# Performance work log

Measured on AMD Instinct MI355X. Metric: run time of the kernel, lower is better.

## Reference

```python
import jax, jax.numpy as jnp
import numpy as np

EMBED = 1024
N_HEAD = 16
D_HID = EMBED // N_HEAD
R_FF = 4
D_FF = EMBED * R_FF
LN_EPS = 1e-5


def layer_norm(x, gamma, beta):
    mu = jnp.mean(x, axis=-1, keepdims=True)
    var = jnp.var(x, axis=-1, keepdims=True)
    return (x - mu) * jax.lax.rsqrt(var + LN_EPS) * gamma + beta


def setup_inputs() -> dict:
    key = jax.random.key(0)
    ks = jax.random.split(key, 10)
    B, S = 4, 2048
    # torch nn.Linear stores weight as [out, in]; y = x @ W.T
    def xavier(k, shape):
        fan_out, fan_in = shape
        lim = np.sqrt(6.0 / (fan_in + fan_out))
        return jax.random.uniform(k, shape, jnp.float32, -lim, lim)
    return {
        "x": jax.random.normal(ks[0], (B, S, EMBED), jnp.float32),
        "Wq": xavier(ks[1], (EMBED, EMBED)),
        "Wk": xavier(ks[2], (EMBED, EMBED)),
        "Wv": xavier(ks[3], (EMBED, EMBED)),
        "Wo": xavier(ks[4], (EMBED, EMBED)),
        "bo": jnp.zeros((EMBED,), jnp.float32),
        "ln1_g": jnp.ones((EMBED,), jnp.float32),
        "ln1_b": jnp.zeros((EMBED,), jnp.float32),
        "ln2_g": jnp.ones((EMBED,), jnp.float32),
        "ln2_b": jnp.zeros((EMBED,), jnp.float32),
        "W1": jax.random.normal(ks[5], (D_FF, EMBED), jnp.float32) * np.sqrt(2.0 / EMBED),
        "b1": jnp.zeros((D_FF,), jnp.float32),
        "W2": xavier(ks[6], (EMBED, D_FF)),
        "b2": jnp.zeros((EMBED,), jnp.float32),
    }


def reference(x, Wq, Wk, Wv, Wo, bo, ln1_g, ln1_b, ln2_g, ln2_b, W1, b1, W2, b2):
    B, S, E = x.shape
    scaling = 1.0 / np.sqrt(D_HID)
    # --- attention (pre-LN), dropout = identity (eval) ---
    xn = layer_norm(x, ln1_g, ln1_b)
    q = (xn @ Wq.T).reshape(B, S, N_HEAD, D_HID) * scaling
    k = (xn @ Wk.T).reshape(B, S, N_HEAD, D_HID)
    v = (xn @ Wv.T).reshape(B, S, N_HEAD, D_HID)
    scores = jnp.einsum("bqhd,bkhd->bhqk", q, k)
    attn = jax.nn.softmax(scores, axis=-1)
    out = jnp.einsum("bhqk,bkhd->bqhd", attn, v).reshape(B, S, E)
    out = out @ Wo.T + bo
    x = x + out
    # --- feed-forward (pre-LN) ---
    xn = layer_norm(x, ln2_g, ln2_b)
    h = jax.nn.relu(xn @ W1.T + b1)
    x = x + (h @ W2.T + b2)
    return x
```

## Files before the change

kernel.cpp:

```cpp
#include <hip/hip_runtime.h>
#include <hip/hip_bf16.h>
#include <cstdint>


typedef __attribute__((ext_vector_type(8))) short bf16x8;
typedef __attribute__((ext_vector_type(4))) float f32x4;

#define LDSAS __attribute__((address_space(3)))
#define GLBAS __attribute__((address_space(1)))

#define CQK 0.18033688011112044f

__device__ __forceinline__ unsigned short f2bf(float f) {
  union { float f; unsigned u; } c; c.f = f;
  unsigned u = c.u + 0x7fffu + ((c.u >> 16) & 1u);
  return (unsigned short)(u >> 16);
}

__device__ __forceinline__ unsigned pk2(float a, float b) {
  __hip_bfloat162 h = __float22bfloat162_rn(make_float2(a, b));
  union { __hip_bfloat162 h; unsigned u; } c; c.h = h; return c.u;
}

__device__ __forceinline__ void async16(const unsigned short* g, unsigned short* l) {
  __builtin_amdgcn_global_load_lds((const GLBAS unsigned int*)g,
                                   (LDSAS unsigned int*)l, 16, 0, 0);
}

__global__ void cvt_all(const float* __restrict__ q, const float* __restrict__ k,
                        const float* __restrict__ v, const float* __restrict__ o,
                        const float* __restrict__ w1, const float* __restrict__ w2,
                        unsigned short* __restrict__ wsb) {
  const long i = (long)blockIdx.x * 256 + threadIdx.x;
  const float* src; unsigned short* dst; long off;
  if (i < 1048576) {
    const long seg = i >> 18, o4 = i & 262143;
    src = (seg == 0) ? q : (seg == 1) ? k : (seg == 2) ? v : o;
    dst = wsb + ((seg == 3) ? 3145728L : seg * 1048576L);
    off = o4;
  } else if (i < 2097152) {
    src = w1; dst = wsb + 4194304; off = i - 1048576;
  } else {
    src = w2; dst = wsb + 8388608; off = i - 2097152;
  }
  const float4 vv = ((const float4*)src)[off];
  ushort4 r;
  r.x = f2bf(vv.x); r.y = f2bf(vv.y); r.z = f2bf(vv.z); r.w = f2bf(vv.w);
  ((ushort4*)dst)[off] = r;
}

__global__ void ln_fwd(const float* __restrict__ x, const float* __restrict__ g,
                       const float* __restrict__ bb, unsigned short* __restrict__ outp) {
  const int row = blockIdx.x, tid = threadIdx.x;
  const float4 v = ((const float4*)(x + (long)row * 1024))[tid];
  float s  = v.x + v.y + v.z + v.w;
  float sq = v.x * v.x + v.y * v.y + v.z * v.z + v.w * v.w;
#pragma unroll
  for (int off = 1; off < 64; off <<= 1) {
    s  += __shfl_xor(s, off);
    sq += __shfl_xor(sq, off);
  }
  __shared__ float red[8];
  const int wv = tid >> 6, lane = tid & 63;
  if (lane == 0) { red[wv] = s; red[4 + wv] = sq; }
  __syncthreads();
  s  = red[0] + red[1] + red[2] + red[3];
  sq = red[4] + red[5] + red[6] + red[7];
  const float mu  = s * (1.f / 1024.f);
  const float var = sq * (1.f / 1024.f) - mu * mu;
  const float rstd = rsqrtf(var + 1e-5f);
  const float4 gv = ((const float4*)g)[tid];
  const float4 bv = ((const float4*)bb)[tid];
  ushort4 o;
  o.x = f2bf((v.x - mu) * rstd * gv.x + bv.x);
  o.y = f2bf((v.y - mu) * rstd * gv.y + bv.y);
  o.z = f2bf((v.z - mu) * rstd * gv.z + bv.z);
  o.w = f2bf((v.w - mu) * rstd * gv.w + bv.w);
  ((ushort4*)(outp + (long)row * 1024))[tid] = o;
}

template <int EPI>
__launch_bounds__(256)
__global__ void gemm_bt(const unsigned short* __restrict__ A,
                        const unsigned short* __restrict__ B,
                        void* __restrict__ Cout,
                        const float* __restrict__ bias,
                        const float* __restrict__ res,
                        int M, int N, int K) {
  __shared__ __align__(16) unsigned short As[128 * 64];
  __shared__ __align__(16) unsigned short Bs[128 * 64];
  const int tid  = threadIdx.x;
  const int lane = tid & 63;
  const int wvu  = __builtin_amdgcn_readfirstlane(tid >> 6);
  const int quad = lane >> 4, l16 = lane & 15;
  const int wm = wvu >> 1, wn = wvu & 1;

  const int gx = gridDim.x;
  const int id = blockIdx.y * gx + blockIdx.x;
  const int xcd = id & 7, slot = id >> 3;
  const int by = xcd * 8 + (slot & 7);
  const int bx = slot >> 3;
  const long m0 = (long)by * 128, n0 = (long)bx * 128;

  f32x4 acc[4][4];
#pragma unroll
  for (int i = 0; i < 4; i++)
#pragma unroll
    for (int j = 0; j < 4; j++) acc[i][j] = (f32x4){0.f, 0.f, 0.f, 0.f};

  const int rxA = l16 & 7;
  const int c0A = quad ^ rxA;
  int srow[4], sgc[4];
#pragma unroll
  for (int j = 0; j < 4; ++j) {
    const int s = wvu * 256 + j * 64 + lane;
    srow[j] = s >> 3;
    sgc[j] = ((s & 7) ^ (srow[j] & 7)) * 8;
  }

  for (int k0 = 0; k0 < K; k0 += 64) {
    __syncthreads();
#pragma unroll
    for (int j = 0; j < 4; ++j) {
      const int db = (wvu * 256 + j * 64) * 8;
      async16(A + (m0 + srow[j]) * K + k0 + sgc[j], As + db);
      async16(B + (n0 + srow[j]) * K + k0 + sgc[j], Bs + db);
    }
    __syncthreads();

#pragma unroll
    for (int kc = 0; kc < 2; ++kc) {
      const int ch = (c0A ^ (kc * 4)) * 8;
      bf16x8 af[4], bfr[4];
#pragma unroll
      for (int t = 0; t < 4; ++t) {
        af[t]  = *(const bf16x8*)(As + (wm * 64 + t * 16 + l16) * 64 + ch);
        bfr[t] = *(const bf16x8*)(Bs + (wn * 64 + t * 16 + l16) * 64 + ch);
      }
#pragma unroll
      for (int mt = 0; mt < 4; ++mt)
#pragma unroll
        for (int nt = 0; nt < 4; ++nt)
          acc[mt][nt] = __builtin_amdgcn_mfma_f32_16x16x32_bf16(af[mt], bfr[nt],
                                                                acc[mt][nt], 0, 0, 0);
    }
  }

#pragma unroll
  for (int nt = 0; nt < 4; ++nt) {
    const long col = n0 + wn * 64 + nt * 16 + l16;
    float bv = 0.f;
    if (EPI == 1 || EPI == 2) bv = bias[col];
    const float scl = (EPI == 3 && col < 1024) ? CQK : 1.0f;
#pragma unroll
    for (int mt = 0; mt < 4; ++mt) {
#pragma unroll
      for (int r = 0; r < 4; ++r) {
        const long row = m0 + wm * 64 + mt * 16 + quad * 4 + r;
        const long idx = row * (long)N + col;
        float v = acc[mt][nt][r];
        if (EPI == 0) {
          ((unsigned short*)Cout)[idx] = f2bf(v);
        } else if (EPI == 1) {
          ((float*)Cout)[idx] = v + bv + res[idx];
        } else if (EPI == 2) {
          v += bv;
          ((unsigned short*)Cout)[idx] = f2bf(v > 0.f ? v : 0.f);
        } else {
          ((unsigned short*)Cout)[idx] = f2bf(v * scl);
        }
      }
    }
  }
}

__global__ void vprep(const unsigned short* __restrict__ qkv,
                      unsigned short* __restrict__ vt) {
  __shared__ unsigned short T[64 * 68];
  const int tid = threadIdx.x;
  const int t = blockIdx.x;
  const int bh = blockIdx.y;
  const int b = bh >> 4, h = bh & 15;
  const long base = ((long)b * 2048 + t * 64) * 3072 + 2048 + h * 64;
#pragma unroll
  for (int i = 0; i < 4; ++i) {
    int c = i * 256 + tid;
    int r = c >> 4, d4 = (c & 15) * 4;
    *(ushort4*)(T + r * 68 + d4) = *(const ushort4*)(qkv + base + (long)r * 3072 + d4);
  }
  __syncthreads();
  unsigned short* out = vt + ((long)bh * 32 + t) * 4096;
#pragma unroll
  for (int i = 0; i < 4; ++i) {
    int u = i * 256 + tid;
    int c = u >> 1, half = u & 1;
    int d = c >> 3;
    int k = ((c & 7) - d) & 7;
    int kvp4 = k * 8 + half * 4;
    int sk = (kvp4 & 32) | ((kvp4 & 4) << 2) | ((kvp4 & 16) >> 1) | ((kvp4 & 8) >> 1);
    ushort4 o;
    o.x = T[(sk + 0) * 68 + d];
    o.y = T[(sk + 1) * 68 + d];
    o.z = T[(sk + 2) * 68 + d];
    o.w = T[(sk + 3) * 68 + d];
    *(ushort4*)(out + u * 4) = o;
  }
}

__launch_bounds__(512, 4)
__global__ void attn_fwd(const unsigned short* __restrict__ qkv,
                         const unsigned short* __restrict__ vt,
                         unsigned short* __restrict__ outp) {
  __shared__ __align__(16) unsigned short Qs[128 * 64];
  __shared__ __align__(16) unsigned short Ks[64 * 64];
  __shared__ __align__(16) unsigned short Vs[64 * 64];

  const int tid = threadIdx.x;
  const int lane = tid & 63;
  const int wv = __builtin_amdgcn_readfirstlane(tid >> 6);
  const int quad = lane >> 4, l16 = lane & 15;
  const int qt = blockIdx.x;
  const int bh = blockIdx.y;
  const int b = bh >> 4, h = bh & 15;
  const long rowbase = (long)b * 2048;
  const int hoff = h * 64;

  {
    const unsigned short* qsrc = qkv + (rowbase + qt * 128) * 3072 + hoff;
#pragma unroll
    for (int j = 0; j < 2; ++j) {
      const int c = j * 512 + wv * 64 + lane;
      const int row = c >> 3;
      const int k = ((c & 7) - row) & 7;
      async16(qsrc + (long)row * 3072 + k * 8, Qs + (j * 512 + wv * 64) * 8);
    }
  }
  __syncthreads();

  const int rot0 = (quad + l16) & 7;
  const int rot1 = rot0 ^ 4;

  const int qrow = wv * 16 + l16;
  const bf16x8 bq0 = *(const bf16x8*)(Qs + qrow * 64 + rot0 * 8);
  const bf16x8 bq1 = *(const bf16x8*)(Qs + qrow * 64 + rot1 * 8);

  const int ck = wv * 64 + lane;
  const int krow = ck >> 3;
  const int kk = ((ck & 7) - krow) & 7;
  const unsigned short* ksrc = qkv + (rowbase + krow) * 3072 + 1024 + hoff + kk * 8;
  const unsigned short* vsrc = vt + (long)bh * 131072 + (long)ck * 8;
  unsigned short* kdst = Ks + wv * 512;
  unsigned short* vdst = Vs + wv * 512;

  f32x4 oacc[4];
#pragma unroll
  for (int i = 0; i < 4; i++) oacc[i] = (f32x4){0.f, 0.f, 0.f, 0.f};
  float l_run = 0.f;

  for (int kt = 0; kt < 32; ++kt) {
    __syncthreads();
    async16(ksrc, kdst);
    async16(vsrc, vdst);
    ksrc += 64 * 3072;
    vsrc += 4096;
    __syncthreads();

    f32x4 sacc[4];
#pragma unroll
    for (int t = 0; t < 4; ++t) {
      const int ar = t * 16 + l16;
      bf16x8 ak0 = *(const bf16x8*)(Ks + ar * 64 + rot0 * 8);
      bf16x8 ak1 = *(const bf16x8*)(Ks + ar * 64 + rot1 * 8);
      sacc[t] = (f32x4){0.f, 0.f, 0.f, 0.f};
      sacc[t] = __builtin_amdgcn_mfma_f32_16x16x32_bf16(ak0, bq0, sacc[t], 0, 0, 0);
      sacc[t] = __builtin_amdgcn_mfma_f32_16x16x32_bf16(ak1, bq1, sacc[t], 0, 0, 0);
    }

    union APU { unsigned u[4]; bf16x8 v; } apu[2];
    float rs = 0.f;
#pragma unroll
    for (int a = 0; a < 2; ++a)
#pragma unroll
      for (int t = 0; t < 2; ++t) {
        const f32x4 s = sacc[a * 2 + t];
        const float p0 = __builtin_amdgcn_exp2f(s[0]);
        const float p1 = __builtin_amdgcn_exp2f(s[1]);
        const float p2 = __builtin_amdgcn_exp2f(s[2]);
        const float p3 = __builtin_amdgcn_exp2f(s[3]);
        rs += (p0 + p1) + (p2 + p3);
        apu[a].u[t * 2 + 0] = pk2(p0, p1);
        apu[a].u[t * 2 + 1] = pk2(p2, p3);
      }
    l_run += rs;

#pragma unroll
    for (int dt = 0; dt < 4; ++dt) {
      const int d = dt * 16 + l16;
      bf16x8 bv0 = *(const bf16x8*)(Vs + d * 64 + rot0 * 8);
      bf16x8 bv1 = *(const bf16x8*)(Vs + d * 64 + rot1 * 8);
      oacc[dt] = __builtin_amdgcn_mfma_f32_16x16x32_bf16(apu[0].v, bv0, oacc[dt], 0, 0, 0);
      oacc[dt] = __builtin_amdgcn_mfma_f32_16x16x32_bf16(apu[1].v, bv1, oacc[dt], 0, 0, 0);
    }
  }

  l_run += __shfl_xor(l_run, 16);
  l_run += __shfl_xor(l_run, 32);
  float linv[4];
#pragma unroll
  for (int r = 0; r < 4; ++r) linv[r] = 1.f / __shfl(l_run, quad * 4 + r);
#pragma unroll
  for (int dt = 0; dt < 4; ++dt)
#pragma unroll
    for (int r = 0; r < 4; ++r) {
      const long row = rowbase + qt * 128 + wv * 16 + quad * 4 + r;
      outp[row * 1024 + hoff + dt * 16 + l16] = f2bf(oacc[dt][r] * linv[r]);
    }
}

extern "C" void kernel_launch(void* const* d_in, const int* in_sizes, int n_in,
                              void* d_out, int out_size, void* d_ws, size_t ws_size,
                              hipStream_t stream) {
  (void)in_sizes; (void)n_in; (void)out_size; (void)ws_size;
  const float* x   = (const float*)d_in[0];
  const float* Wq  = (const float*)d_in[1];
  const float* Wk  = (const float*)d_in[2];
  const float* Wv  = (const float*)d_in[3];
  const float* Wo  = (const float*)d_in[4];
  const float* bo  = (const float*)d_in[5];
  const float* g1  = (const float*)d_in[6];
  const float* be1 = (const float*)d_in[7];
  const float* g2  = (const float*)d_in[8];
  const float* be2 = (const float*)d_in[9];
  const float* W1  = (const float*)d_in[10];
  const float* bf1 = (const float*)d_in[11];
  const float* W2  = (const float*)d_in[12];
  const float* bf2 = (const float*)d_in[13];

  char* ws = (char*)d_ws;
  unsigned short* wqkv  = (unsigned short*)(ws);
  unsigned short* wo    = (unsigned short*)(ws + 6291456);
  unsigned short* w1    = (unsigned short*)(ws + 8388608);
  unsigned short* w2    = (unsigned short*)(ws + 16777216);
  unsigned short* xn    = (unsigned short*)(ws + 25165824);
  unsigned short* big   = (unsigned short*)(ws + 41943040);
  unsigned short* attnb = (unsigned short*)(ws + 109051904);
  float*          x1    = (float*)(ws + 125829120);
  unsigned short* vtg   = xn;

  cvt_all<<<12288, 256, 0, stream>>>(Wq, Wk, Wv, Wo, W1, W2, wqkv);

  ln_fwd<<<8192, 256, 0, stream>>>(x, g1, be1, xn);
  gemm_bt<3><<<dim3(24, 64), 256, 0, stream>>>(xn, wqkv, big, nullptr, nullptr,
                                               8192, 3072, 1024);
  vprep<<<dim3(32, 64), 256, 0, stream>>>(big, vtg);
  attn_fwd<<<dim3(16, 64), 512, 0, stream>>>(big, vtg, attnb);
  gemm_bt<1><<<dim3(8, 64), 256, 0, stream>>>(attnb, wo, x1, bo, x,
                                              8192, 1024, 1024);
  ln_fwd<<<8192, 256, 0, stream>>>(x1, g2, be2, xn);
  gemm_bt<2><<<dim3(32, 64), 256, 0, stream>>>(xn, w1, big, bf1, nullptr,
                                               8192, 4096, 1024);
  gemm_bt<1><<<dim3(8, 64), 256, 0, stream>>>(big, w2, (float*)d_out, bf2, x1,
                                              8192, 1024, 4096);
}
```

Before: 524.5 us.

## Restructure attention to 4 waves with 32 query rows each and 128-key tiles

The attention kernel now uses 256 threads, and each wave handles two 16-row query slices, so every K/V fragment read from LDS feeds two MFMAs. Keys are processed in 128-wide tiles, which halves the number of loop iterations and barriers. The softmax row sum is now computed with an MFMA against a ones vector, replacing the scalar adds and shuffles. Blocks are remapped so heads are grouped per XCD for L2 locality, and the GEMM gets a minimum-occupancy launch bound of 3 waves, which may limit registers. In exchange, register and LDS use per block grow, and parallelism per block drops.

```diff
diff --git a/kernel.cpp b/kernel.cpp
--- a/kernel.cpp
+++ b/kernel.cpp
@@ -80,7 +80,7 @@
 }
 
 template <int EPI>
-__launch_bounds__(256)
+__launch_bounds__(256, 3)
 __global__ void gemm_bt(const unsigned short* __restrict__ A,
                         const unsigned short* __restrict__ B,
                         void* __restrict__ Cout,
@@ -207,20 +207,23 @@
   }
 }
 
-__launch_bounds__(512, 4)
+__launch_bounds__(256, 3)
 __global__ void attn_fwd(const unsigned short* __restrict__ qkv,
                          const unsigned short* __restrict__ vt,
                          unsigned short* __restrict__ outp) {
   __shared__ __align__(16) unsigned short Qs[128 * 64];
-  __shared__ __align__(16) unsigned short Ks[64 * 64];
-  __shared__ __align__(16) unsigned short Vs[64 * 64];
+  __shared__ __align__(16) unsigned short Ks[128 * 64];
+  __shared__ __align__(16) unsigned short Vs[128 * 64];
 
   const int tid = threadIdx.x;
   const int lane = tid & 63;
   const int wv = __builtin_amdgcn_readfirstlane(tid >> 6);
   const int quad = lane >> 4, l16 = lane & 15;
-  const int qt = blockIdx.x;
-  const int bh = blockIdx.y;
+
+  const int id = blockIdx.y * 16 + blockIdx.x;
+  const int xcd = id & 7, slot = id >> 3;
+  const int bh = xcd * 8 + (slot >> 4);
+  const int qt = slot & 15;
   const int b = bh >> 4, h = bh & 15;
   const long rowbase = (long)b * 2048;
   const int hoff = h * 64;
@@ -228,11 +231,11 @@
   {
     const unsigned short* qsrc = qkv + (rowbase + qt * 128) * 3072 + hoff;
 #pragma unroll
-    for (int j = 0; j < 2; ++j) {
-      const int c = j * 512 + wv * 64 + lane;
+    for (int j = 0; j < 4; ++j) {
+      const int c = j * 256 + wv * 64 + lane;
       const int row = c >> 3;
       const int k = ((c & 7) - row) & 7;
-      async16(qsrc + (long)row * 3072 + k * 8, Qs + (j * 512 + wv * 64) * 8);
+      async16(qsrc + (long)row * 3072 + k * 8, Qs + (j * 256 + wv * 64) * 8);
     }
   }
   __syncthreads();
@@ -240,81 +243,105 @@
   const int rot0 = (quad + l16) & 7;
   const int rot1 = rot0 ^ 4;
 
-  const int qrow = wv * 16 + l16;
-  const bf16x8 bq0 = *(const bf16x8*)(Qs + qrow * 64 + rot0 * 8);
-  const bf16x8 bq1 = *(const bf16x8*)(Qs + qrow * 64 + rot1 * 8);
-
-  const int ck = wv * 64 + lane;
-  const int krow = ck >> 3;
-  const int kk = ((ck & 7) - krow) & 7;
-  const unsigned short* ksrc = qkv + (rowbase + krow) * 3072 + 1024 + hoff + kk * 8;
-  const unsigned short* vsrc = vt + (long)bh * 131072 + (long)ck * 8;
+  bf16x8 bq[2][2];
+#pragma unroll
+  for (int s = 0; s < 2; ++s) {
+    const int qrow = wv * 32 + s * 16 + l16;
+    bq[s][0] = *(const bf16x8*)(Qs + qrow * 64 + rot0 * 8);
+    bq[s][1] = *(const bf16x8*)(Qs + qrow * 64 + rot1 * 8);
+  }
+
+  const int c0 = wv * 64 + lane;
+  const int r0 = c0 >> 3;
+  const int ks = ((c0 & 7) - r0) & 7;
+  const unsigned short* kptr = qkv + (rowbase + r0) * 3072 + 1024 + hoff + ks * 8;
+  const unsigned short* vptr = vt + (long)bh * 131072 + (long)c0 * 8;
   unsigned short* kdst = Ks + wv * 512;
   unsigned short* vdst = Vs + wv * 512;
 
-  f32x4 oacc[4];
-#pragma unroll
-  for (int i = 0; i < 4; i++) oacc[i] = (f32x4){0.f, 0.f, 0.f, 0.f};
-  float l_run = 0.f;
-
-  for (int kt = 0; kt < 32; ++kt) {
+  bf16x8 ones;
+#pragma unroll
+  for (int i = 0; i < 8; ++i) ones[i] = (short)0x3F80;
+
+  f32x4 oacc[2][4], lacc[2];
+#pragma unroll
+  for (int s = 0; s < 2; ++s) {
+    lacc[s] = (f32x4){0.f, 0.f, 0.f, 0.f};
+#pragma unroll
+    for (int i = 0; i < 4; ++i) oacc[s][i] = (f32x4){0.f, 0.f, 0.f, 0.f};
+  }
+
+  for (int kt = 0; kt < 16; ++kt) {
     __syncthreads();
-    async16(ksrc, kdst);
-    async16(vsrc, vdst);
-    ksrc += 64 * 3072;
-    vsrc += 4096;
+#pragma unroll
+    for (int j = 0; j < 4; ++j) {
+      async16(kptr + (long)j * 32 * 3072, kdst + j * 2048);
+      async16(vptr + j * 2048, vdst + j * 2048);
+    }
+    kptr += (long)128 * 3072;
+    vptr += 8192;
     __syncthreads();
 
-    f32x4 sacc[4];
-#pragma unroll
-    for (int t = 0; t < 4; ++t) {
+    f32x4 sacc[2][8];
+#pragma unroll
+    for (int t = 0; t < 8; ++t) {
       const int ar = t * 16 + l16;
       bf16x8 ak0 = *(const bf16x8*)(Ks + ar * 64 + rot0 * 8);
       bf16x8 ak1 = *(const bf16x8*)(Ks + ar * 64 + rot1 * 8);
-      sacc[t] = (f32x4){0.f, 0.f, 0.f, 0.f};
-      sacc[t] = __builtin_amdgcn_mfma_f32_16x16x32_bf16(ak0, bq0, sacc[t], 0, 0, 0);
-      sacc[t] = __builtin_amdgcn_mfma_f32_16x16x32_bf16(ak1, bq1, sacc[t], 0, 0, 0);
-    }
-
-    union APU { unsigned u[4]; bf16x8 v; } apu[2];
-    float rs = 0.f;
-#pragma unroll
-    for (int a = 0; a < 2; ++a)
-#pragma unroll
-      for (int t = 0; t < 2; ++t) {
-        const f32x4 s = sacc[a * 2 + t];
-        const float p0 = __builtin_amdgcn_exp2f(s[0]);
-        const float p1 = __builtin_amdgcn_exp2f(s[1]);
-        const float p2 = __builtin_amdgcn_exp2f(s[2]);
-        const float p3 = __builtin_amdgcn_exp2f(s[3]);
-        rs += (p0 + p1) + (p2 + p3);
-        apu[a].u[t * 2 + 0] = pk2(p0, p1);
-        apu[a].u[t * 2 + 1] = pk2(p2, p3);
-      }
-    l_run += rs;
-
-#pragma unroll
-    for (int dt = 0; dt < 4; ++dt) {
-      const int d = dt * 16 + l16;
-      bf16x8 bv0 = *(const bf16x8*)(Vs + d * 64 + rot0 * 8);
-      bf16x8 bv1 = *(const bf16x8*)(Vs + d * 64 + rot1 * 8);
-      oacc[dt] = __builtin_amdgcn_mfma_f32_16x16x32_bf16(apu[0].v, bv0, oacc[dt], 0, 0, 0);
-      oacc[dt] = __builtin_amdgcn_mfma_f32_16x16x32_bf16(apu[1].v, bv1, oacc[dt], 0, 0, 0);
-    }
-  }
-
-  l_run += __shfl_xor(l_run, 16);
-  l_run += __shfl_xor(l_run, 32);
-  float linv[4];
-#pragma unroll
-  for (int r = 0; r < 4; ++r) linv[r] = 1.f / __shfl(l_run, quad * 4 + r);
-#pragma unroll
-  for (int dt = 0; dt < 4; ++dt)
-#pragma unroll
-    for (int r = 0; r < 4; ++r) {
-      const long row = rowbase + qt * 128 + wv * 16 + quad * 4 + r;
-      outp[row * 1024 + hoff + dt * 16 + l16] = f2bf(oacc[dt][r] * linv[r]);
-    }
+#pragma unroll
+      for (int s = 0; s < 2; ++s) {
+        f32x4 z = (f32x4){0.f, 0.f, 0.f, 0.f};
+        z = __builtin_amdgcn_mfma_f32_16x16x32_bf16(ak0, bq[s][0], z, 0, 0, 0);
+        sacc[s][t] = __builtin_amdgcn_mfma_f32_16x16x32_bf16(ak1, bq[s][1], z, 0, 0, 0);
+      }
+    }
+
+    union APU { unsigned u[4]; bf16x8 v; } ap[2][4];
+#pragma unroll
+    for (int s = 0; s < 2; ++s)
+#pragma unroll
+      for (int hf = 0; hf < 4; ++hf) {
+#pragma unroll
+        for (int t = 0; t < 2; ++t) {
+          const f32x4 sv = sacc[s][hf * 2 + t];
+          const float p0 = __builtin_amdgcn_exp2f(sv[0]);
+          const float p1 = __builtin_amdgcn_exp2f(sv[1]);
+          const float p2 = __builtin_amdgcn_exp2f(sv[2]);
+          const float p3 = __builtin_amdgcn_exp2f(sv[3]);
+          ap[s][hf].u[t * 2 + 0] = pk2(p0, p1);
+          ap[s][hf].u[t * 2 + 1] = pk2(p2, p3);
+        }
+        lacc[s] = __builtin_amdgcn_mfma_f32_16x16x32_bf16(ap[s][hf].v, ones,
+                                                          lacc[s], 0, 0, 0);
+      }
+
+#pragma unroll
+    for (int hf = 0; hf < 4; ++hf) {
+      const int vbase = (hf >> 1) * 4096 + ((hf & 1) ? rot1 : rot0) * 8;
+#pragma unroll
+      for (int dt = 0; dt < 4; ++dt) {
+        bf16x8 bv = *(const bf16x8*)(Vs + vbase + (dt * 16 + l16) * 64);
+#pragma unroll
+        for (int s = 0; s < 2; ++s)
+          oacc[s][dt] = __builtin_amdgcn_mfma_f32_16x16x32_bf16(ap[s][hf].v, bv,
+                                                                oacc[s][dt], 0, 0, 0);
+      }
+    }
+  }
+
+#pragma unroll
+  for (int s = 0; s < 2; ++s) {
+    float linv[4];
+#pragma unroll
+    for (int r = 0; r < 4; ++r) linv[r] = 1.f / lacc[s][r];
+#pragma unroll
+    for (int dt = 0; dt < 4; ++dt)
+#pragma unroll
+      for (int r = 0; r < 4; ++r) {
+        const long row = rowbase + qt * 128 + wv * 32 + s * 16 + quad * 4 + r;
+        outp[row * 1024 + hoff + dt * 16 + l16] = f2bf(oacc[s][dt][r] * linv[r]);
+      }
+  }
 }
 
 extern "C" void kernel_launch(void* const* d_in, const int* in_sizes, int n_in,
@@ -353,7 +380,7 @@
   gemm_bt<3><<<dim3(24, 64), 256, 0, stream>>>(xn, wqkv, big, nullptr, nullptr,
                                                8192, 3072, 1024);
   vprep<<<dim3(32, 64), 256, 0, stream>>>(big, vtg);
-  attn_fwd<<<dim3(16, 64), 512, 0, stream>>>(big, vtg, attnb);
+  attn_fwd<<<dim3(16, 64), 256, 0, stream>>>(big, vtg, attnb);
   gemm_bt<1><<<dim3(8, 64), 256, 0, stream>>>(attnb, wo, x1, bo, x,
                                               8192, 1024, 1024);
   ln_fwd<<<8192, 256, 0, stream>>>(x1, g2, be2, xn);
```

After: 491.6 us. 6.3% less time.
